# Kernel optimization log

Hardware: AMD Instinct MI355X
Metric: run time of the kernel (lower is better)

Reference implementation:

```python
import jax, jax.numpy as jnp
import numpy as np


def setup_inputs() -> dict:
    key = jax.random.key(0)
    k1, k2 = jax.random.split(key)
    B, C, H, W = 16, 256, 64, 64
    K, D = 1024, 256
    z = jax.random.normal(k1, (B, C, H, W), dtype=jnp.float32)
    embedding = jax.random.normal(k2, (K, D), dtype=jnp.float32)
    return {"z": z, "embedding": embedding}


def reference(z, embedding):
    # _preprocess: shift channel dim (axis 1) to last, flatten -> [N, D]
    B, C, H, W = z.shape
    encoded_permuted = jnp.transpose(z, (0, 2, 3, 1))  # [B, H, W, C]
    permuted_shape = encoded_permuted.shape
    encoded_flat = encoded_permuted.reshape(-1, C)  # [N, D]

    x_sq = jnp.sum(encoded_flat * encoded_flat, axis=1, keepdims=True)  # [N, 1]
    e_sq = jnp.sum(embedding * embedding, axis=1)  # [K]
    cross = encoded_flat @ embedding.T  # [N, K]
    distances = x_sq - 2.0 * cross + e_sq[None, :]
    codebook_indices = jnp.argmin(distances, axis=1)  # [N]
    quantized_lookup = embedding[codebook_indices]  # [N, D]

    # straight-through estimator
    quantized_flat = encoded_flat + jax.lax.stop_gradient(quantized_lookup - encoded_flat)

    # _postprocess: reshape and shift last dim back to axis 1
    quantized = jnp.transpose(quantized_flat.reshape(permuted_shape), (0, 3, 1, 2))
    return (encoded_flat, quantized_flat, codebook_indices, quantized)
```

## Files before the change

### kernel.cpp

```cpp
#include <hip/hip_runtime.h>
#include <hip/hip_bf16.h>

typedef _Float16 h8 __attribute__((ext_vector_type(8)));
typedef float f4 __attribute__((ext_vector_type(4)));

#define N_TOK 65536
#define DIM 256
#define KCODES 1024
#define HWSZ 4096

__device__ __forceinline__ void gll16(const void* g, void* l) {
    __builtin_amdgcn_global_load_lds((const __attribute__((address_space(1))) void*)g,
                                     (__attribute__((address_space(3))) void*)l, 16, 0, 0);
}


__global__ void k_prep_frag(const float* __restrict__ emb, _Float16* __restrict__ BhF,
                            _Float16* __restrict__ BlF) {
    int gi = blockIdx.x * 256 + threadIdx.x;
    int kb = gi >> 9, s = (gi >> 6) & 7, dq = (gi >> 4) & 3, r = gi & 15;
    int code = kb * 16 + r;
    const float* src = emb + (size_t)code * DIM + s * 32 + dq * 8;
    float4 x0 = *(const float4*)(src);
    float4 x1 = *(const float4*)(src + 4);
    float xs[8] = {x0.x, x0.y, x0.z, x0.w, x1.x, x1.y, x1.z, x1.w};
    h8 hi, lo;
#pragma unroll
    for (int j = 0; j < 8; ++j) {
        _Float16 h = (_Float16)xs[j];
        hi[j] = h;
        lo[j] = (_Float16)(xs[j] - (float)h);
    }
    *(h8*)(BhF + (size_t)gi * 8) = hi;
    *(h8*)(BlF + (size_t)gi * 8) = lo;
}

__global__ void k_esq(const float* __restrict__ emb, float* __restrict__ e_sq) {
    int t = threadIdx.x;
    int code = blockIdx.x * 4 + (t >> 6);
    int l = t & 63;
    float4 v = *(const float4*)(emb + (size_t)code * DIM + l * 4);
    float s = v.x * v.x + v.y * v.y + v.z * v.z + v.w * v.w;
#pragma unroll
    for (int off = 32; off >= 1; off >>= 1) s += __shfl_xor(s, off);
    if (l == 0) e_sq[code] = s;
}

__global__ void k_transpose(const float* __restrict__ z, float* __restrict__ enc,
                            _Float16* __restrict__ AhF, _Float16* __restrict__ AlF) {
    __shared__ float T[64][65];
    int blk = blockIdx.x;
    int b = blk >> 8;
    int rem = blk & 255;
    int c0 = (rem >> 6) * 64;
    int hw0 = (rem & 63) * 64;
    int t = threadIdx.x;
    const float* zp = z + (size_t)b * DIM * HWSZ;
    {
        int hw4 = (t & 15) * 4, cl = t >> 4;
#pragma unroll
        for (int i = 0; i < 4; ++i) {
            int c = cl + i * 16;
            float4 v = *(const float4*)(zp + (size_t)(c0 + c) * HWSZ + hw0 + hw4);
            T[c][hw4 + 0] = v.x; T[c][hw4 + 1] = v.y;
            T[c][hw4 + 2] = v.z; T[c][hw4 + 3] = v.w;
        }
    }
    __syncthreads();
    {
        int c4 = (t & 15) * 4, hwl = t >> 4;
#pragma unroll
        for (int i = 0; i < 4; ++i) {
            int hw = hwl + i * 16;
            float4 v;
            v.x = T[c4 + 0][hw]; v.y = T[c4 + 1][hw];
            v.z = T[c4 + 2][hw]; v.w = T[c4 + 3][hw];
            *(float4*)(enc + (size_t)(b * HWSZ + hw0 + hw) * DIM + c0 + c4) = v;
        }
    }
    {
        int base_nb = b * 256 + (hw0 >> 4);
#pragma unroll
        for (int i = 0; i < 2; ++i) {
            int gidx = i * 256 + t;
            int nbi = gidx >> 7, si = (gidx >> 6) & 1, dq = (gidx >> 4) & 3, r = gidx & 15;
            int hwl = nbi * 16 + r;
            int cl = si * 32 + dq * 8;
            h8 hi, lo;
#pragma unroll
            for (int j = 0; j < 8; ++j) {
                float x = T[cl + j][hwl];
                _Float16 h = (_Float16)x;
                hi[j] = h;
                lo[j] = (_Float16)(x - (float)h);
            }
            size_t G = (((size_t)(base_nb + nbi) * 8) + (c0 >> 5) + si) * 64 + dq * 16 + r;
            *(h8*)(AhF + G * 8) = hi;
            *(h8*)(AlF + G * 8) = lo;
        }
    }
}

#define WAITV(n) asm volatile("s_waitcnt vmcnt(" #n ")" ::: "memory")
#define BARRIER __builtin_amdgcn_s_barrier()
#define PRIO1 __builtin_amdgcn_s_setprio(1)
#define PRIO0 __builtin_amdgcn_s_setprio(0)
#define LGKM0 asm volatile("s_waitcnt lgkmcnt(0)" ::: "memory")
#define SGB0 __builtin_amdgcn_sched_barrier(0)

extern __shared__ char SB[];

__global__ __launch_bounds__(512, 2)
void k_gemm_argmin(const _Float16* __restrict__ AhF, const _Float16* __restrict__ AlF,
                   const _Float16* __restrict__ BhF, const _Float16* __restrict__ BlF,
                   const float* __restrict__ e_sq,
                   float* __restrict__ pV1, int* __restrict__ pI1) {
    int gid = blockIdx.x;
    int grp = gid >> 7;
    int colTile = (gid >> 5) & 3;
    int rowTile = grp * 32 + (gid & 31);
    int r0 = rowTile * 256, c0 = colTile * 256;
    int t = threadIdx.x;
    int w = t >> 6, l = t & 63;
    int wm = w >> 2, wn = w & 3;
    int l16 = l & 15, lhi = l >> 4;

    const char* gAh = (const char*)AhF + (((size_t)(rowTile * 16 + 2 * w)) << 13) + (l << 4);
    const char* gAl = (const char*)AlF + (((size_t)(rowTile * 16 + 2 * w)) << 13) + (l << 4);
    const char* gBh = (const char*)BhF + (((size_t)(colTile * 16 + 2 * w)) << 13) + (l << 4);
    const char* gBl = (const char*)BlF + (((size_t)(colTile * 16 + 2 * w)) << 13) + (l << 4);

#define ISSUE_A(c) do { const char* a_ = (((c) >> 3) == 2) ? gAl : gAh; \
    char* bp_ = SB + ((c) & 3) * 32768 + ((2 * w) << 10); \
    const int so_ = ((c) & 7) << 10; \
    gll16(a_ + so_, bp_); gll16(a_ + 8192 + so_, bp_ + 1024); } while (0)

#define ISSUE_B(c) do { const char* b_ = (((c) >> 3) == 1) ? gBl : gBh; \
    char* bp_ = SB + ((c) & 3) * 32768 + 16384 + ((2 * w) << 10); \
    const int so_ = ((c) & 7) << 10; \
    gll16(b_ + so_, bp_); gll16(b_ + 8192 + so_, bp_ + 1024); } while (0)

#define RD_A(c, mo) { const char* bp_ = SB + ((c) & 3) * 32768; \
    _Pragma("unroll") for (int mf = 0; mf < 4; ++mf) \
        ah[mf] = *(const h8*)(bp_ + ((wm * 8 + (mo) + mf) << 10) + (l << 4)); }

#define RD_B(c) { const char* bp_ = SB + ((c) & 3) * 32768 + 16384; \
    _Pragma("unroll") for (int nf = 0; nf < 4; ++nf) \
        bh[nf] = *(const h8*)(bp_ + ((wn * 4 + nf) << 10) + (l << 4)); }

#define MFMA_HALF(mo) { _Pragma("unroll") for (int mf = 0; mf < 4; ++mf) \
    _Pragma("unroll") for (int nf = 0; nf < 4; ++nf) \
        acc[(mo) + mf][nf] = __builtin_amdgcn_mfma_f32_16x16x32_f16(ah[mf], bh[nf], acc[(mo) + mf][nf], 0, 0, 0); }

#define CHUNK(c, W) \
    WAITV(W); BARRIER; \
    if ((c) <= 20) { ISSUE_A((c) + 3); } \
    RD_A(c, 0); RD_B(c); \
    LGKM0; SGB0; PRIO1; MFMA_HALF(0); PRIO0; \
    BARRIER; \
    if ((c) <= 20) { ISSUE_B((c) + 3); } \
    RD_A(c, 4); \
    LGKM0; SGB0; PRIO1; MFMA_HALF(4); PRIO0;

    f4 acc[8][4];
#pragma unroll
    for (int i = 0; i < 8; ++i)
#pragma unroll
        for (int j = 0; j < 4; ++j) acc[i][j] = (f4)0.0f;

    h8 ah[4], bh[4];

    ISSUE_A(0); ISSUE_B(0); ISSUE_A(1); ISSUE_B(1); ISSUE_A(2); ISSUE_B(2);

    CHUNK(0, 8)   CHUNK(1, 8)   CHUNK(2, 8)   CHUNK(3, 8)
    CHUNK(4, 8)   CHUNK(5, 8)   CHUNK(6, 8)   CHUNK(7, 8)
    CHUNK(8, 8)   CHUNK(9, 8)   CHUNK(10, 8)  CHUNK(11, 8)
    CHUNK(12, 8)  CHUNK(13, 8)  CHUNK(14, 8)  CHUNK(15, 8)
    CHUNK(16, 8)  CHUNK(17, 8)  CHUNK(18, 8)  CHUNK(19, 8)
    CHUNK(20, 8)  CHUNK(21, 8)  CHUNK(22, 4)  CHUNK(23, 0)

    float* smV = (float*)SB;
    int* smI = (int*)(SB + 4096);

    float esq[4];
#pragma unroll
    for (int nf = 0; nf < 4; ++nf) esq[nf] = e_sq[c0 + wn * 64 + nf * 16 + l16];

#pragma unroll
    for (int mf = 0; mf < 8; ++mf) {
#pragma unroll
        for (int rg = 0; rg < 4; ++rg) {
            float bestV = 3.4e38f;
            int bestI = 0;
#pragma unroll
            for (int nf = 0; nf < 4; ++nf) {
                float v = esq[nf] - 2.0f * acc[mf][nf][rg];
                int ci = c0 + wn * 64 + nf * 16 + l16;
                if (v < bestV || (v == bestV && ci < bestI)) { bestV = v; bestI = ci; }
            }
#pragma unroll
            for (int off = 1; off < 16; off <<= 1) {
                float vv = __shfl_xor(bestV, off);
                int ii = __shfl_xor(bestI, off);
                if (vv < bestV || (vv == bestV && ii < bestI)) { bestV = vv; bestI = ii; }
            }
            if (l16 == 0) {
                int rloc = wm * 128 + mf * 16 + lhi * 4 + rg;
                smV[wn * 256 + rloc] = bestV;
                smI[wn * 256 + rloc] = bestI;
            }
        }
    }
    __syncthreads();
    if (t < 256) {
        float bestV = smV[t];
        int bestI = smI[t];
#pragma unroll
        for (int wn2 = 1; wn2 < 4; ++wn2) {
            float v = smV[wn2 * 256 + t];
            int i2 = smI[wn2 * 256 + t];
            if (v < bestV || (v == bestV && i2 < bestI)) { bestV = v; bestI = i2; }
        }
        pV1[colTile * N_TOK + r0 + t] = bestV;
        pI1[colTile * N_TOK + r0 + t] = bestI;
    }
}

__global__ void k_final_all(const float* __restrict__ pV1, const int* __restrict__ pI1,
                            const float* __restrict__ emb,
                            float* __restrict__ out2, float* __restrict__ out1,
                            float* __restrict__ out3) {
    __shared__ int sidx[256];
    __shared__ float E[32][257];
    int t = threadIdx.x;
    int n0 = blockIdx.x * 256;
    int n = n0 + t;
    float v1 = pV1[n];
    int i1 = pI1[n];
#pragma unroll
    for (int ct = 1; ct < 4; ++ct) {
        float a1 = pV1[ct * N_TOK + n];
        int ai = pI1[ct * N_TOK + n];
        if (a1 < v1 || (a1 == v1 && ai < i1)) { v1 = a1; i1 = ai; }
    }
    out2[n] = (float)i1;
    sidx[t] = i1;
    __syncthreads();
    {
        int rr = t >> 2, q = t & 3;
#pragma unroll
        for (int i = 0; i < 4; ++i) {
            int r = i * 64 + rr;
            int idx = sidx[r];
            const float* src = emb + (size_t)idx * DIM + q * 64;
            float* dst = out1 + (size_t)(n0 + r) * DIM + q * 64;
#pragma unroll
            for (int j = 0; j < 16; ++j)
                *(float4*)(dst + j * 4) = *(const float4*)(src + j * 4);
        }
    }
    int b = n0 >> 12;
    int hw0b = n0 & 4095;
    for (int sub = 0; sub < 8; ++sub) {
        __syncthreads();
        {
            int r = t >> 3, oct = t & 7;
            int idx = sidx[sub * 32 + r];
            const float* src = emb + (size_t)idx * DIM + oct * 32;
#pragma unroll
            for (int i = 0; i < 8; ++i) {
                float4 v = *(const float4*)(src + i * 4);
                E[r][oct * 32 + i * 4 + 0] = v.x;
                E[r][oct * 32 + i * 4 + 1] = v.y;
                E[r][oct * 32 + i * 4 + 2] = v.z;
                E[r][oct * 32 + i * 4 + 3] = v.w;
            }
        }
        __syncthreads();
        {
            int w = t >> 6, l = t & 63;
            int ch = l >> 5, hw = l & 31;
            float* dst = out3 + (size_t)b * DIM * HWSZ + hw0b + sub * 32 + hw;
#pragma unroll
            for (int it = 0; it < 32; ++it) {
                int c = w * 64 + it * 2 + ch;
                dst[(size_t)c * HWSZ] = E[hw][c];
            }
        }
    }
}

extern "C" void kernel_launch(void* const* d_in, const int* in_sizes, int n_in,
                              void* d_out, int out_size, void* d_ws, size_t ws_size,
                              hipStream_t stream) {
    const float* z = (const float*)d_in[0];
    const float* emb = (const float*)d_in[1];
    float* out = (float*)d_out;
    float* out0 = out;
    float* out1 = out + 16777216;
    float* out2 = out + 33554432;
    float* out3 = out + 33619968;

    _Float16* AhF = (_Float16*)out1;
    _Float16* AlF = (_Float16*)(out1 + 8388608);

    char* ws = (char*)d_ws;
    _Float16* BhF = (_Float16*)(ws);
    _Float16* BlF = (_Float16*)(ws + 524288);
    float* e_sq = (float*)(ws + 1048576);
    float* pV1 = (float*)(ws + 1052672);
    int* pI1 = (int*)(ws + 2101248);

    hipFuncSetAttribute((const void*)k_gemm_argmin,
                        hipFuncAttributeMaxDynamicSharedMemorySize, 131072);

    k_prep_frag<<<128, 256, 0, stream>>>(emb, BhF, BlF);
    k_esq<<<256, 256, 0, stream>>>(emb, e_sq);
    k_transpose<<<4096, 256, 0, stream>>>(z, out0, AhF, AlF);
    k_gemm_argmin<<<1024, 512, 131072, stream>>>(AhF, AlF, BhF, BlF, e_sq, pV1, pI1);
    k_final_all<<<256, 256, 0, stream>>>(pV1, pI1, emb, out2, out1, out3);
}
```

Measured before the change: 222.3 us.

## Deepen GEMM LDS ring to five stages with register double-buffered fragments

Restructures the main GEMM loop. The LDS ring grows from four to five stages, so loads are issued four chunks ahead, and the A and B tile loads are merged into one issue per chunk. The next chunk's full A and B fragments are read into a second register set while the current chunk's 32 MFMAs run, which replaces two barriers per chunk with one. This aims to hide LDS read latency and cut synchronisation overhead. In exchange it uses 160KB of dynamic LDS and roughly doubles fragment register use, which risks spills under the existing launch bounds.

```diff
diff --git a/kernel.cpp b/kernel.cpp
--- a/kernel.cpp
+++ b/kernel.cpp
@@ -102,10 +102,10 @@
 }
 
 #define WAITV(n) asm volatile("s_waitcnt vmcnt(" #n ")" ::: "memory")
+#define LGKM(n) asm volatile("s_waitcnt lgkmcnt(" #n ")" ::: "memory")
 #define BARRIER __builtin_amdgcn_s_barrier()
 #define PRIO1 __builtin_amdgcn_s_setprio(1)
 #define PRIO0 __builtin_amdgcn_s_setprio(0)
-#define LGKM0 asm volatile("s_waitcnt lgkmcnt(0)" ::: "memory")
 #define SGB0 __builtin_amdgcn_sched_barrier(0)
 
 extern __shared__ char SB[];
@@ -130,37 +130,33 @@
     const char* gBh = (const char*)BhF + (((size_t)(colTile * 16 + 2 * w)) << 13) + (l << 4);
     const char* gBl = (const char*)BlF + (((size_t)(colTile * 16 + 2 * w)) << 13) + (l << 4);
 
-#define ISSUE_A(c) do { const char* a_ = (((c) >> 3) == 2) ? gAl : gAh; \
-    char* bp_ = SB + ((c) & 3) * 32768 + ((2 * w) << 10); \
+#define ISSUE(c) do { \
+    const char* a_ = (((c) >> 3) == 2) ? gAl : gAh; \
+    const char* b_ = (((c) >> 3) == 1) ? gBl : gBh; \
     const int so_ = ((c) & 7) << 10; \
-    gll16(a_ + so_, bp_); gll16(a_ + 8192 + so_, bp_ + 1024); } while (0)
-
-#define ISSUE_B(c) do { const char* b_ = (((c) >> 3) == 1) ? gBl : gBh; \
-    char* bp_ = SB + ((c) & 3) * 32768 + 16384 + ((2 * w) << 10); \
-    const int so_ = ((c) & 7) << 10; \
-    gll16(b_ + so_, bp_); gll16(b_ + 8192 + so_, bp_ + 1024); } while (0)
-
-#define RD_A(c, mo) { const char* bp_ = SB + ((c) & 3) * 32768; \
-    _Pragma("unroll") for (int mf = 0; mf < 4; ++mf) \
-        ah[mf] = *(const h8*)(bp_ + ((wm * 8 + (mo) + mf) << 10) + (l << 4)); }
-
-#define RD_B(c) { const char* bp_ = SB + ((c) & 3) * 32768 + 16384; \
+    char* sp_ = SB + ((c) % 5) * 32768; \
+    gll16(a_ + so_, sp_ + ((2 * w) << 10)); \
+    gll16(a_ + 8192 + so_, sp_ + ((2 * w + 1) << 10)); \
+    gll16(b_ + so_, sp_ + 16384 + ((2 * w) << 10)); \
+    gll16(b_ + 8192 + so_, sp_ + 16384 + ((2 * w + 1) << 10)); \
+} while (0)
+
+#define READ(c, aX, bX) { const char* bp_ = SB + ((c) % 5) * 32768; \
+    _Pragma("unroll") for (int mf = 0; mf < 8; ++mf) \
+        aX[mf] = *(const h8*)(bp_ + ((wm * 8 + mf) << 10) + (l << 4)); \
     _Pragma("unroll") for (int nf = 0; nf < 4; ++nf) \
-        bh[nf] = *(const h8*)(bp_ + ((wn * 4 + nf) << 10) + (l << 4)); }
-
-#define MFMA_HALF(mo) { _Pragma("unroll") for (int mf = 0; mf < 4; ++mf) \
+        bX[nf] = *(const h8*)(bp_ + 16384 + ((wn * 4 + nf) << 10) + (l << 4)); }
+
+#define MFMA32(A_, B_) { _Pragma("unroll") for (int mf = 0; mf < 8; ++mf) \
     _Pragma("unroll") for (int nf = 0; nf < 4; ++nf) \
-        acc[(mo) + mf][nf] = __builtin_amdgcn_mfma_f32_16x16x32_f16(ah[mf], bh[nf], acc[(mo) + mf][nf], 0, 0, 0); }
-
-#define CHUNK(c, W) \
-    WAITV(W); BARRIER; \
-    if ((c) <= 20) { ISSUE_A((c) + 3); } \
-    RD_A(c, 0); RD_B(c); \
-    LGKM0; SGB0; PRIO1; MFMA_HALF(0); PRIO0; \
-    BARRIER; \
-    if ((c) <= 20) { ISSUE_B((c) + 3); } \
-    RD_A(c, 4); \
-    LGKM0; SGB0; PRIO1; MFMA_HALF(4); PRIO0;
+        acc[mf][nf] = __builtin_amdgcn_mfma_f32_16x16x32_f16(A_[mf], B_[nf], acc[mf][nf], 0, 0, 0); }
+
+#define CHUNK(c, AC, BC, AN, BN, WV, LG) \
+    if ((c) < 23) { READ((c) + 1, AN, BN); } \
+    if ((c) < 20) { ISSUE((c) + 4); } \
+    LGKM(LG); SGB0; \
+    PRIO1; MFMA32(AC, BC); PRIO0; \
+    WAITV(WV); BARRIER;
 
     f4 acc[8][4];
 #pragma unroll
@@ -168,16 +164,24 @@
 #pragma unroll
         for (int j = 0; j < 4; ++j) acc[i][j] = (f4)0.0f;
 
-    h8 ah[4], bh[4];
-
-    ISSUE_A(0); ISSUE_B(0); ISSUE_A(1); ISSUE_B(1); ISSUE_A(2); ISSUE_B(2);
-
-    CHUNK(0, 8)   CHUNK(1, 8)   CHUNK(2, 8)   CHUNK(3, 8)
-    CHUNK(4, 8)   CHUNK(5, 8)   CHUNK(6, 8)   CHUNK(7, 8)
-    CHUNK(8, 8)   CHUNK(9, 8)   CHUNK(10, 8)  CHUNK(11, 8)
-    CHUNK(12, 8)  CHUNK(13, 8)  CHUNK(14, 8)  CHUNK(15, 8)
-    CHUNK(16, 8)  CHUNK(17, 8)  CHUNK(18, 8)  CHUNK(19, 8)
-    CHUNK(20, 8)  CHUNK(21, 8)  CHUNK(22, 4)  CHUNK(23, 0)
+    h8 aA[8], bA[4], aB[8], bB[4];
+
+    ISSUE(0); ISSUE(1); ISSUE(2); ISSUE(3);
+    WAITV(8); BARRIER;
+    READ(0, aA, bA);
+
+    CHUNK(0, aA, bA, aB, bB, 8, 12)   CHUNK(1, aB, bB, aA, bA, 8, 12)
+    CHUNK(2, aA, bA, aB, bB, 8, 12)   CHUNK(3, aB, bB, aA, bA, 8, 12)
+    CHUNK(4, aA, bA, aB, bB, 8, 12)   CHUNK(5, aB, bB, aA, bA, 8, 12)
+    CHUNK(6, aA, bA, aB, bB, 8, 12)   CHUNK(7, aB, bB, aA, bA, 8, 12)
+    CHUNK(8, aA, bA, aB, bB, 8, 12)   CHUNK(9, aB, bB, aA, bA, 8, 12)
+    CHUNK(10, aA, bA, aB, bB, 8, 12)  CHUNK(11, aB, bB, aA, bA, 8, 12)
+    CHUNK(12, aA, bA, aB, bB, 8, 12)  CHUNK(13, aB, bB, aA, bA, 8, 12)
+    CHUNK(14, aA, bA, aB, bB, 8, 12)  CHUNK(15, aB, bB, aA, bA, 8, 12)
+    CHUNK(16, aA, bA, aB, bB, 8, 12)  CHUNK(17, aB, bB, aA, bA, 8, 12)
+    CHUNK(18, aA, bA, aB, bB, 8, 12)  CHUNK(19, aB, bB, aA, bA, 8, 12)
+    CHUNK(20, aA, bA, aB, bB, 4, 12)  CHUNK(21, aB, bB, aA, bA, 0, 12)
+    CHUNK(22, aA, bA, aB, bB, 0, 12)  CHUNK(23, aB, bB, aA, bA, 0, 0)
 
     float* smV = (float*)SB;
     int* smI = (int*)(SB + 4096);
@@ -312,11 +316,11 @@
     int* pI1 = (int*)(ws + 2101248);
 
     hipFuncSetAttribute((const void*)k_gemm_argmin,
-                        hipFuncAttributeMaxDynamicSharedMemorySize, 131072);
+                        hipFuncAttributeMaxDynamicSharedMemorySize, 163840);
 
     k_prep_frag<<<128, 256, 0, stream>>>(emb, BhF, BlF);
     k_esq<<<256, 256, 0, stream>>>(emb, e_sq);
     k_transpose<<<4096, 256, 0, stream>>>(z, out0, AhF, AlF);
-    k_gemm_argmin<<<1024, 512, 131072, stream>>>(AhF, AlF, BhF, BlF, e_sq, pV1, pI1);
+    k_gemm_argmin<<<1024, 512, 163840, stream>>>(AhF, AlF, BhF, BlF, e_sq, pV1, pI1);
     k_final_all<<<256, 256, 0, stream>>>(pV1, pI1, emb, out2, out1, out3);
 }
```

New measurement: 278.2 us. +25.1%, slower.
